# Performance work log

Measured on AMD Instinct MI355X. Metric: run time of the kernel, lower is better.

Reference implementation:

```python
import jax, jax.numpy as jnp
from jax import lax
import numpy as np

B, N, H, K = 64, 256, 1024, 3  # batch, num_proposals, hidden_dim, conv kernel size
LN_EPS = 1e-5


def setup_inputs() -> dict:
    key = jax.random.key(0)
    k1, k2, k3 = jax.random.split(key, 3)
    scale = 1.0 / np.sqrt(H)
    return {
        "f": jax.random.normal(k1, (B, N, H), dtype=jnp.float32),
        "k": jax.random.normal(k2, (B, N, H), dtype=jnp.float32),
        "W_lin": jax.random.normal(k3, (N * K, H), dtype=jnp.float32) * scale,
        "b_lin": jnp.zeros((N * K,), dtype=jnp.float32),
        "ln_gamma": jnp.ones((H,), dtype=jnp.float32),
        "ln_beta": jnp.zeros((H,), dtype=jnp.float32),
    }


def _conv_one(x, w):
    # x: [N, H] (channels, length); w: [N_out, N_in, K]
    # PyTorch F.conv1d is cross-correlation, same as lax conv with no flip.
    y = lax.conv_general_dilated(
        x[None], w, window_strides=(1,), padding="SAME",
        dimension_numbers=("NCH", "OIH", "NCH"))
    return y[0]  # [N, H]


def reference(f, k, W_lin, b_lin, ln_gamma, ln_beta):
    # Dynamic weight generation: [B, N, H] -> [B, N, N*K] -> [B, N, N, K]
    weight = jnp.einsum("bnh,oh->bno", f, W_lin) + b_lin
    weight = weight.reshape(B, N, N, K)
    # Per-sample dynamic conv1d over the hidden dim (batched via vmap)
    out = jax.vmap(_conv_one)(k, weight)  # [B, N, H]
    # LayerNorm over hidden dim
    mu = jnp.mean(out, axis=-1, keepdims=True)
    var = jnp.var(out, axis=-1, keepdims=True)
    out = (out - mu) * lax.rsqrt(var + LN_EPS) * ln_gamma + ln_beta
    return out
```

## Files before the change

kernel.cpp:

```cpp
#include <hip/hip_runtime.h>
#include <math.h>

#define Bsz 64
#define Nn  256
#define Hh  1024
#define NK  768

typedef __bf16 bf16;
typedef bf16 bf16x4 __attribute__((ext_vector_type(4)));
typedef bf16 bf16x8 __attribute__((ext_vector_type(8)));
typedef float floatx4 __attribute__((ext_vector_type(4)));

#define KT_ROWS   1026
#define KT_BSTRIDE (KT_ROWS * 256)

__device__ __forceinline__ void gl_lds16(const bf16* g, bf16* l) {
    __builtin_amdgcn_global_load_lds(
        (__attribute__((address_space(1))) void*)(g),
        (__attribute__((address_space(3))) void*)(l), 16, 0, 0);
}
__device__ __forceinline__ void gl_lds16f(const float* g, float* l) {
    __builtin_amdgcn_global_load_lds(
        (__attribute__((address_space(1))) void*)(g),
        (__attribute__((address_space(3))) void*)(l), 16, 0, 0);
}

__global__ __launch_bounds__(256) void transpose_kernel(
    const float* __restrict__ kin, bf16* __restrict__ kTp)
{
    __shared__ float Tf[64 * 128];
    const int tid = threadIdx.x;
    const int bid = blockIdx.x;
    const int hb = bid & 7, ib = (bid >> 3) & 3, b = bid >> 5;
    const int i0 = ib * 64, h0 = hb * 128;
    const float* src = kin + ((size_t)b << 18);
    bf16* dstb = kTp + (size_t)b * KT_BSTRIDE;

    if (hb == 0 && ib == 0) {
        dstb[tid] = (bf16)0.f;
        dstb[(size_t)1025 * 256 + tid] = (bf16)0.f;
    }
    #pragma unroll
    for (int j = 0; j < 8; ++j) {
        int c  = tid + j * 256;
        int il = c >> 5;
        int hq = (c & 31) ^ j;
        gl_lds16f(src + (size_t)(i0 + il) * Hh + h0 + hq * 4, Tf + c * 4);
    }
    __syncthreads();
    const int q = tid & 7;
    #pragma unroll
    for (int p = 0; p < 4; ++p) {
        int hl = (tid >> 3) + p * 32;
        bf16x8 o;
        #pragma unroll
        for (int j = 0; j < 8; ++j) {
            int i = q * 8 + j;
            float v = Tf[i * 128 + (((hl >> 2) ^ q) << 2) + (hl & 3)];
            o[j] = (bf16)v;
        }
        *(bf16x8*)&dstb[(size_t)(h0 + hl + 1) * 256 + i0 + q * 8] = o;
    }
}

__global__ __launch_bounds__(256) void cast_kernel(
    const float* __restrict__ f, const float* __restrict__ wl,
    bf16* __restrict__ fbf, bf16* __restrict__ wlbf)
{
    const int STR = 524288;
    const int u0  = blockIdx.x * 256 + threadIdx.x;
    float4 a[8];
    #pragma unroll
    for (int k = 0; k < 4; ++k) {
        const float4* s4 = (const float4*)f + ((size_t)(u0 + k * STR) * 2);
        a[2 * k]     = s4[0];
        a[2 * k + 1] = s4[1];
    }
    float4 b0, b1;
    const bool doW = (u0 < 98304);
    if (doW) {
        const float4* s4 = (const float4*)wl + ((size_t)u0 * 2);
        b0 = s4[0];
        b1 = s4[1];
    }
    __builtin_amdgcn_sched_barrier(0);
    #pragma unroll
    for (int k = 0; k < 4; ++k) {
        bf16x8 o = {(bf16)a[2*k].x, (bf16)a[2*k].y, (bf16)a[2*k].z, (bf16)a[2*k].w,
                    (bf16)a[2*k+1].x, (bf16)a[2*k+1].y, (bf16)a[2*k+1].z, (bf16)a[2*k+1].w};
        ((bf16x8*)fbf)[u0 + k * STR] = o;
    }
    if (doW) {
        bf16x8 o = {(bf16)b0.x, (bf16)b0.y, (bf16)b0.z, (bf16)b0.w,
                    (bf16)b1.x, (bf16)b1.y, (bf16)b1.z, (bf16)b1.w};
        ((bf16x8*)wlbf)[u0] = o;
    }
}

__global__ __launch_bounds__(256) void gemm1_mfma(
    const bf16* __restrict__ A,
    const bf16* __restrict__ Bw,
    const float* __restrict__ bias,
    bf16* __restrict__ wgt3)
{
    __shared__ bf16 smem[25600];
    bf16* As = smem;
    bf16* Bs = smem + 8192;
    const int tid  = threadIdx.x;
    const int wave = tid >> 6, lane = tid & 63;
    const int row0 = blockIdx.y * 128;
    const int col0 = blockIdx.x * 192;

    const bf16* gA[4]; bf16* lA[4];
    #pragma unroll
    for (int j = 0; j < 4; ++j) {
        int s = tid + j * 256;
        int reg = s >> 9, rem = s & 511, row = rem >> 2, quad = rem & 3;
        gA[j] = A + (size_t)(row0 + row) * Hh + reg * 32 + quad * 8;
        lA[j] = As + s * 8;
    }
    const bf16* gB[6]; bf16* lB[6];
    #pragma unroll
    for (int j = 0; j < 6; ++j) {
        int s = tid + j * 256;
        int reg = s / 768, rem = s - reg * 768, row = rem >> 2, quad = rem & 3;
        gB[j] = Bw + (size_t)(col0 + row) * Hh + reg * 32 + quad * 8;
        lB[j] = Bs + s * 8;
    }

    const int wm = wave & 1, wn = wave >> 1;
    const int fm = lane & 15, koct = (lane >> 4) * 8;

    floatx4 zero = {0.f, 0.f, 0.f, 0.f};
    floatx4 acc[4][6];
    #pragma unroll
    for (int i = 0; i < 4; ++i)
        #pragma unroll
        for (int j = 0; j < 6; ++j) acc[i][j] = zero;

    for (int k0 = 0; k0 < Hh; k0 += 64) {
        #pragma unroll
        for (int j = 0; j < 4; ++j) gl_lds16(gA[j] + k0, lA[j]);
        #pragma unroll
        for (int j = 0; j < 6; ++j) gl_lds16(gB[j] + k0, lB[j]);
        __syncthreads();
        #pragma unroll
        for (int q = 0; q < 2; ++q) {
            bf16x8 af[4], bfr[6];
            #pragma unroll
            for (int mt = 0; mt < 4; ++mt)
                af[mt] = *(const bf16x8*)&As[q * 4096 + (wm * 64 + mt * 16 + fm) * 32 + koct];
            #pragma unroll
            for (int nt = 0; nt < 6; ++nt)
                bfr[nt] = *(const bf16x8*)&Bs[q * 6144 + (wn * 96 + nt * 16 + fm) * 32 + koct];
            #pragma unroll
            for (int mt = 0; mt < 4; ++mt)
                #pragma unroll
                for (int nt = 0; nt < 6; ++nt)
                    acc[mt][nt] = __builtin_amdgcn_mfma_f32_16x16x32_bf16(
                        af[mt], bfr[nt], acc[mt][nt], 0, 0, 0);
        }
        __syncthreads();
    }

    const int b  = row0 >> 8;
    const int nb = row0 & 255;
    bf16* Cs = smem;
    #pragma unroll
    for (int nt = 0; nt < 6; ++nt) {
        int c = wn * 96 + nt * 16 + fm;
        float bl = bias[col0 + c];
        #pragma unroll
        for (int mt = 0; mt < 4; ++mt) {
            int rb = wm * 64 + mt * 16 + (lane >> 4) * 4;
            #pragma unroll
            for (int r = 0; r < 4; ++r)
                Cs[(rb + r) * 200 + c] = (bf16)(acc[mt][nt][r] + bl);
        }
    }
    __syncthreads();
    const int i0 = blockIdx.x * 64;
    #pragma unroll
    for (int j = 0; j < 12; ++j) {
        int s = tid + j * 256;
        int t = s >> 10, rem = s & 1023, n = rem >> 3, q8 = rem & 7;
        bf16x8 v;
        #pragma unroll
        for (int u = 0; u < 8; ++u)
            v[u] = Cs[n * 200 + (q8 * 8 + u) * 3 + t];
        *(bf16x8*)&wgt3[((size_t)(b * 3 + t) << 16) + ((size_t)(nb + n) << 8) + i0 + q8 * 8] = v;
    }
}

__global__ __launch_bounds__(256, 3) void conv_mfma(
    const bf16* __restrict__ kTp,
    const bf16* __restrict__ wgt3,
    bf16* __restrict__ cbuf)
{
    __shared__ bf16 As[6144];
    __shared__ bf16 Ks[8256];
    const int tid  = threadIdx.x;
    const int wave = tid >> 6, lane = tid & 63;
    const int b  = blockIdx.z;
    const int o0 = blockIdx.y * 64;
    const int h0 = blockIdx.x * 256;
    const int wm = wave & 1, wn = wave >> 1;
    const int fm = lane & 15, koct = (lane >> 4) * 8;

    const bf16* gA[3]; bf16* lA[3];
    #pragma unroll
    for (int j = 0; j < 3; ++j) {
        int s = tid + j * 256;
        int t = s >> 8, rem = s & 255, o = rem >> 2, iq = rem & 3;
        gA[j] = wgt3 + ((size_t)(b * 3 + t) << 16) + ((size_t)(o0 + o) << 8) + iq * 8;
        lA[j] = As + s * 8;
    }
    const bf16* kb = kTp + (size_t)b * KT_BSTRIDE;
    const bf16* gK[4]; bf16* lK[4];
    #pragma unroll
    for (int j = 0; j < 4; ++j) {
        int s = tid + j * 256;
        int r = s >> 2, quad = s & 3;
        gK[j] = kb + (size_t)(h0 + r) * 256 + quad * 8;
        lK[j] = Ks + s * 8;
    }

    floatx4 zero = {0.f, 0.f, 0.f, 0.f};
    floatx4 acc[2][8];
    #pragma unroll
    for (int i = 0; i < 2; ++i)
        #pragma unroll
        for (int j = 0; j < 8; ++j) acc[i][j] = zero;

    for (int ic = 0; ic < 8; ++ic) {
        const int i0 = ic * 32;
        __syncthreads();
        #pragma unroll
        for (int j = 0; j < 3; ++j) gl_lds16(gA[j] + i0, lA[j]);
        #pragma unroll
        for (int j = 0; j < 4; ++j) gl_lds16(gK[j] + i0, lK[j]);
        if (tid < 8) {
            int r = 256 + (tid >> 2), q = tid & 3;
            bf16x8 v = *(const bf16x8*)&kb[(size_t)(h0 + r) * 256 + i0 + q * 8];
            *(bf16x8*)&Ks[r * 32 + q * 8] = v;
        }
        __syncthreads();
        #pragma unroll
        for (int t = 0; t < 3; ++t) {
            bf16x8 af[2], bfr[8];
            #pragma unroll
            for (int mt = 0; mt < 2; ++mt)
                af[mt] = *(const bf16x8*)&As[t * 2048 + (wm * 32 + mt * 16 + fm) * 32 + koct];
            #pragma unroll
            for (int nt = 0; nt < 8; ++nt)
                bfr[nt] = *(const bf16x8*)&Ks[(wn * 128 + nt * 16 + fm + t) * 32 + koct];
            #pragma unroll
            for (int mt = 0; mt < 2; ++mt)
                #pragma unroll
                for (int nt = 0; nt < 8; ++nt)
                    acc[mt][nt] = __builtin_amdgcn_mfma_f32_16x16x32_bf16(
                        af[mt], bfr[nt], acc[mt][nt], 0, 0, 0);
        }
    }

    #pragma unroll
    for (int mt = 0; mt < 2; ++mt) {
        int o = o0 + wm * 32 + mt * 16 + (lane >> 4) * 4;
        #pragma unroll
        for (int nt = 0; nt < 8; ++nt) {
            int h = h0 + wn * 128 + nt * 16 + fm;
            #pragma unroll
            for (int r = 0; r < 4; ++r)
                cbuf[((size_t)(b * 256 + o + r) << 10) + h] = (bf16)acc[mt][nt][r];
        }
    }
}

__global__ __launch_bounds__(256) void ln_kernel(
    const bf16* __restrict__ cbuf, const float* __restrict__ gamma,
    const float* __restrict__ beta, float* __restrict__ out)
{
    const int tid  = threadIdx.x;
    const int t    = tid & 127;
    const int half = tid >> 7;
    bf16x8 v[4];
    #pragma unroll
    for (int it = 0; it < 4; ++it) {
        const int row = (blockIdx.x << 3) + it * 2 + half;
        v[it] = *(const bf16x8*)(cbuf + ((size_t)row << 10) + t * 8);
    }
    float4 g0  = ((const float4*)gamma)[t * 2];
    float4 g1  = ((const float4*)gamma)[t * 2 + 1];
    float4 be0 = ((const float4*)beta)[t * 2];
    float4 be1 = ((const float4*)beta)[t * 2 + 1];
    __shared__ float r1[2][4], r2[2][4];
    #pragma unroll
    for (int it = 0; it < 4; ++it) {
        const int row = (blockIdx.x << 3) + it * 2 + half;
        float x[8];
        float s1 = 0.f, s2 = 0.f;
        #pragma unroll
        for (int u = 0; u < 8; ++u) {
            x[u] = (float)v[it][u];
            s1 += x[u];
            s2 += x[u] * x[u];
        }
        #pragma unroll
        for (int m = 1; m < 64; m <<= 1) {
            s1 += __shfl_xor(s1, m, 64);
            s2 += __shfl_xor(s2, m, 64);
        }
        const int p = it & 1;
        if ((tid & 63) == 0) { r1[p][tid >> 6] = s1; r2[p][tid >> 6] = s2; }
        __syncthreads();
        float S1 = r1[p][2 * half] + r1[p][2 * half + 1];
        float S2 = r2[p][2 * half] + r2[p][2 * half + 1];
        float mu   = S1 * (1.0f / 1024.0f);
        float var  = S2 * (1.0f / 1024.0f) - mu * mu;
        float rstd = rsqrtf(var + 1e-5f);
        float4 o0, o1;
        o0.x = (x[0] - mu) * rstd * g0.x + be0.x;
        o0.y = (x[1] - mu) * rstd * g0.y + be0.y;
        o0.z = (x[2] - mu) * rstd * g0.z + be0.z;
        o0.w = (x[3] - mu) * rstd * g0.w + be0.w;
        o1.x = (x[4] - mu) * rstd * g1.x + be1.x;
        o1.y = (x[5] - mu) * rstd * g1.y + be1.y;
        o1.z = (x[6] - mu) * rstd * g1.z + be1.z;
        o1.w = (x[7] - mu) * rstd * g1.w + be1.w;
        float* orow = out + ((size_t)row << 10) + t * 8;
        ((float4*)orow)[0] = o0;
        ((float4*)orow)[1] = o1;
    }
}

extern "C" void kernel_launch(void* const* d_in, const int* in_sizes, int n_in,
                              void* d_out, int out_size, void* d_ws, size_t ws_size,
                              hipStream_t stream) {
    const float* f     = (const float*)d_in[0];
    const float* kin   = (const float*)d_in[1];
    const float* W_lin = (const float*)d_in[2];
    const float* b_lin = (const float*)d_in[3];
    const float* gamma = (const float*)d_in[4];
    const float* beta  = (const float*)d_in[5];
    float* out = (float*)d_out;

    char* ws = (char*)d_ws;
    bf16* fbf  = (bf16*)(ws);
    bf16* cbuf = (bf16*)(ws);
    bf16* wlbf = (bf16*)(ws + 33554432);
    bf16* kTp  = (bf16*)(ws + 35127296);
    bf16* wgt3 = (bf16*)(ws + 68747264);

    transpose_kernel<<<2048, 256, 0, stream>>>(kin, kTp);
    cast_kernel<<<2048, 256, 0, stream>>>(f, W_lin, fbf, wlbf);
    gemm1_mfma<<<dim3(4, 128), 256, 0, stream>>>(fbf, wlbf, b_lin, wgt3);
    conv_mfma<<<dim3(4, 4, 64), 256, 0, stream>>>(kTp, wgt3, cbuf);
    ln_kernel<<<2048, 256, 0, stream>>>(cbuf, gamma, beta, out);
}
```

Before: 274.9 us.

## Double-buffer LDS tiles in gemm1 and conv kernels to overlap loads with MFMA

Both the weight-generation GEMM and the dynamic conv kernel now use two LDS buffers. The next K-slice is prefetched with global_load_lds while MFMAs run on the current one, which leaves one barrier per iteration instead of two. The GEMM K step shrinks from 64 to 32 to fit two buffers in the existing shared array. The conv kernel doubles its LDS, lowers its occupancy hint from 3 to 2 blocks, and prefetches its halo rows through registers. Lower occupancy and more loop iterations could offset the overlap gain.

```diff
diff --git a/kernel.cpp b/kernel.cpp
--- a/kernel.cpp
+++ b/kernel.cpp
@@ -104,28 +104,26 @@
     bf16* __restrict__ wgt3)
 {
     __shared__ bf16 smem[25600];
-    bf16* As = smem;
-    bf16* Bs = smem + 8192;
     const int tid  = threadIdx.x;
     const int wave = tid >> 6, lane = tid & 63;
     const int row0 = blockIdx.y * 128;
     const int col0 = blockIdx.x * 192;
 
-    const bf16* gA[4]; bf16* lA[4];
-    #pragma unroll
-    for (int j = 0; j < 4; ++j) {
-        int s = tid + j * 256;
-        int reg = s >> 9, rem = s & 511, row = rem >> 2, quad = rem & 3;
-        gA[j] = A + (size_t)(row0 + row) * Hh + reg * 32 + quad * 8;
-        lA[j] = As + s * 8;
-    }
-    const bf16* gB[6]; bf16* lB[6];
-    #pragma unroll
-    for (int j = 0; j < 6; ++j) {
-        int s = tid + j * 256;
-        int reg = s / 768, rem = s - reg * 768, row = rem >> 2, quad = rem & 3;
-        gB[j] = Bw + (size_t)(col0 + row) * Hh + reg * 32 + quad * 8;
-        lB[j] = Bs + s * 8;
+    const bf16* gA[2]; int lA[2];
+    #pragma unroll
+    for (int j = 0; j < 2; ++j) {
+        int s = tid + j * 256;
+        int row = s >> 2, quad = s & 3;
+        gA[j] = A + (size_t)(row0 + row) * Hh + quad * 8;
+        lA[j] = s * 8;
+    }
+    const bf16* gB[3]; int lB[3];
+    #pragma unroll
+    for (int j = 0; j < 3; ++j) {
+        int s = tid + j * 256;
+        int row = s >> 2, quad = s & 3;
+        gB[j] = Bw + (size_t)(col0 + row) * Hh + quad * 8;
+        lB[j] = 4096 + s * 8;
     }
 
     const int wm = wave & 1, wn = wave >> 1;
@@ -138,29 +136,38 @@
         #pragma unroll
         for (int j = 0; j < 6; ++j) acc[i][j] = zero;
 
-    for (int k0 = 0; k0 < Hh; k0 += 64) {
-        #pragma unroll
-        for (int j = 0; j < 4; ++j) gl_lds16(gA[j] + k0, lA[j]);
-        #pragma unroll
-        for (int j = 0; j < 6; ++j) gl_lds16(gB[j] + k0, lB[j]);
+    #pragma unroll
+    for (int j = 0; j < 2; ++j) gl_lds16(gA[j], &smem[lA[j]]);
+    #pragma unroll
+    for (int j = 0; j < 3; ++j) gl_lds16(gB[j], &smem[lB[j]]);
+    __syncthreads();
+
+    int cur = 0;
+    for (int hs = 0; hs < 32; ++hs) {
+        if (hs < 31) {
+            const int ko = (hs + 1) * 32;
+            const int nb = (cur ^ 1) * 10240;
+            #pragma unroll
+            for (int j = 0; j < 2; ++j) gl_lds16(gA[j] + ko, &smem[nb + lA[j]]);
+            #pragma unroll
+            for (int j = 0; j < 3; ++j) gl_lds16(gB[j] + ko, &smem[nb + lB[j]]);
+        }
+        const int cb = cur * 10240;
+        bf16x8 af[4], bfr[6];
+        #pragma unroll
+        for (int mt = 0; mt < 4; ++mt)
+            af[mt] = *(const bf16x8*)&smem[cb + (wm * 64 + mt * 16 + fm) * 32 + koct];
+        #pragma unroll
+        for (int nt = 0; nt < 6; ++nt)
+            bfr[nt] = *(const bf16x8*)&smem[cb + 4096 + (wn * 96 + nt * 16 + fm) * 32 + koct];
+        #pragma unroll
+        for (int mt = 0; mt < 4; ++mt)
+            #pragma unroll
+            for (int nt = 0; nt < 6; ++nt)
+                acc[mt][nt] = __builtin_amdgcn_mfma_f32_16x16x32_bf16(
+                    af[mt], bfr[nt], acc[mt][nt], 0, 0, 0);
         __syncthreads();
-        #pragma unroll
-        for (int q = 0; q < 2; ++q) {
-            bf16x8 af[4], bfr[6];
-            #pragma unroll
-            for (int mt = 0; mt < 4; ++mt)
-                af[mt] = *(const bf16x8*)&As[q * 4096 + (wm * 64 + mt * 16 + fm) * 32 + koct];
-            #pragma unroll
-            for (int nt = 0; nt < 6; ++nt)
-                bfr[nt] = *(const bf16x8*)&Bs[q * 6144 + (wn * 96 + nt * 16 + fm) * 32 + koct];
-            #pragma unroll
-            for (int mt = 0; mt < 4; ++mt)
-                #pragma unroll
-                for (int nt = 0; nt < 6; ++nt)
-                    acc[mt][nt] = __builtin_amdgcn_mfma_f32_16x16x32_bf16(
-                        af[mt], bfr[nt], acc[mt][nt], 0, 0, 0);
-        }
-        __syncthreads();
+        cur ^= 1;
     }
 
     const int b  = row0 >> 8;
@@ -192,13 +199,13 @@
     }
 }
 
-__global__ __launch_bounds__(256, 3) void conv_mfma(
+__global__ __launch_bounds__(256, 2) void conv_mfma(
     const bf16* __restrict__ kTp,
     const bf16* __restrict__ wgt3,
     bf16* __restrict__ cbuf)
 {
-    __shared__ bf16 As[6144];
-    __shared__ bf16 Ks[8256];
+    __shared__ bf16 As[2][6144];
+    __shared__ bf16 Ks[2][8256];
     const int tid  = threadIdx.x;
     const int wave = tid >> 6, lane = tid & 63;
     const int b  = blockIdx.z;
@@ -207,23 +214,25 @@
     const int wm = wave & 1, wn = wave >> 1;
     const int fm = lane & 15, koct = (lane >> 4) * 8;
 
-    const bf16* gA[3]; bf16* lA[3];
+    const bf16* gA[3]; int lA[3];
     #pragma unroll
     for (int j = 0; j < 3; ++j) {
         int s = tid + j * 256;
         int t = s >> 8, rem = s & 255, o = rem >> 2, iq = rem & 3;
         gA[j] = wgt3 + ((size_t)(b * 3 + t) << 16) + ((size_t)(o0 + o) << 8) + iq * 8;
-        lA[j] = As + s * 8;
+        lA[j] = s * 8;
     }
     const bf16* kb = kTp + (size_t)b * KT_BSTRIDE;
-    const bf16* gK[4]; bf16* lK[4];
+    const bf16* gK[4]; int lK[4];
     #pragma unroll
     for (int j = 0; j < 4; ++j) {
         int s = tid + j * 256;
         int r = s >> 2, quad = s & 3;
         gK[j] = kb + (size_t)(h0 + r) * 256 + quad * 8;
-        lK[j] = Ks + s * 8;
-    }
+        lK[j] = s * 8;
+    }
+    const bf16* gH = kb + (size_t)(h0 + 256 + (tid >> 2)) * 256 + (tid & 3) * 8;
+    const int lH = (256 + (tid >> 2)) * 32 + (tid & 3) * 8;
 
     floatx4 zero = {0.f, 0.f, 0.f, 0.f};
     floatx4 acc[2][8];
@@ -232,28 +241,35 @@
         #pragma unroll
         for (int j = 0; j < 8; ++j) acc[i][j] = zero;
 
+    bf16x8 hv;
+    if (tid < 8) hv = *(const bf16x8*)gH;
+    #pragma unroll
+    for (int j = 0; j < 3; ++j) gl_lds16(gA[j], &As[0][lA[j]]);
+    #pragma unroll
+    for (int j = 0; j < 4; ++j) gl_lds16(gK[j], &Ks[0][lK[j]]);
+    if (tid < 8) *(bf16x8*)&Ks[0][lH] = hv;
+    __syncthreads();
+
+    int cur = 0;
     for (int ic = 0; ic < 8; ++ic) {
-        const int i0 = ic * 32;
-        __syncthreads();
-        #pragma unroll
-        for (int j = 0; j < 3; ++j) gl_lds16(gA[j] + i0, lA[j]);
-        #pragma unroll
-        for (int j = 0; j < 4; ++j) gl_lds16(gK[j] + i0, lK[j]);
-        if (tid < 8) {
-            int r = 256 + (tid >> 2), q = tid & 3;
-            bf16x8 v = *(const bf16x8*)&kb[(size_t)(h0 + r) * 256 + i0 + q * 8];
-            *(bf16x8*)&Ks[r * 32 + q * 8] = v;
-        }
-        __syncthreads();
+        const int nxo = (ic + 1) * 32;
+        bf16x8 hn;
+        if (ic < 7) {
+            if (tid < 8) hn = *(const bf16x8*)(gH + nxo);
+            #pragma unroll
+            for (int j = 0; j < 3; ++j) gl_lds16(gA[j] + nxo, &As[cur ^ 1][lA[j]]);
+            #pragma unroll
+            for (int j = 0; j < 4; ++j) gl_lds16(gK[j] + nxo, &Ks[cur ^ 1][lK[j]]);
+        }
         #pragma unroll
         for (int t = 0; t < 3; ++t) {
             bf16x8 af[2], bfr[8];
             #pragma unroll
             for (int mt = 0; mt < 2; ++mt)
-                af[mt] = *(const bf16x8*)&As[t * 2048 + (wm * 32 + mt * 16 + fm) * 32 + koct];
+                af[mt] = *(const bf16x8*)&As[cur][t * 2048 + (wm * 32 + mt * 16 + fm) * 32 + koct];
             #pragma unroll
             for (int nt = 0; nt < 8; ++nt)
-                bfr[nt] = *(const bf16x8*)&Ks[(wn * 128 + nt * 16 + fm + t) * 32 + koct];
+                bfr[nt] = *(const bf16x8*)&Ks[cur][(wn * 128 + nt * 16 + fm + t) * 32 + koct];
             #pragma unroll
             for (int mt = 0; mt < 2; ++mt)
                 #pragma unroll
@@ -261,6 +277,9 @@
                     acc[mt][nt] = __builtin_amdgcn_mfma_f32_16x16x32_bf16(
                         af[mt], bfr[nt], acc[mt][nt], 0, 0, 0);
         }
+        if (ic < 7 && tid < 8) *(bf16x8*)&Ks[cur ^ 1][lH] = hn;
+        __syncthreads();
+        cur ^= 1;
     }
 
     #pragma unroll
```

Result: no change. 274.3 us (-0.2%).

## Fuse fp32-to-bf16 cast into GEMM loads and remap grids for XCD locality

Applied to the files above, without the earlier changes.

Removes the separate cast kernel. The GEMM now loads fp32 f and W_lin directly into registers, converts them to bf16 and stores them to LDS, which saves a full write and re-read of the bf16 copies. Both the GEMM and the conv kernels switch to a 1-D grid with XCD-aware block remapping so blocks sharing a batch land on the same XCD and reuse its L2. The conv tile in h is halved, with fewer accumulators and the occupancy hint dropped, which gives more blocks. The cost is that the direct-to-LDS async loads become synchronous register loads with no double buffering in the GEMM.

```diff
diff --git a/kernel.cpp b/kernel.cpp
--- a/kernel.cpp
+++ b/kernel.cpp
@@ -63,69 +63,33 @@
     }
 }
 
-__global__ __launch_bounds__(256) void cast_kernel(
-    const float* __restrict__ f, const float* __restrict__ wl,
-    bf16* __restrict__ fbf, bf16* __restrict__ wlbf)
-{
-    const int STR = 524288;
-    const int u0  = blockIdx.x * 256 + threadIdx.x;
-    float4 a[8];
-    #pragma unroll
-    for (int k = 0; k < 4; ++k) {
-        const float4* s4 = (const float4*)f + ((size_t)(u0 + k * STR) * 2);
-        a[2 * k]     = s4[0];
-        a[2 * k + 1] = s4[1];
-    }
-    float4 b0, b1;
-    const bool doW = (u0 < 98304);
-    if (doW) {
-        const float4* s4 = (const float4*)wl + ((size_t)u0 * 2);
-        b0 = s4[0];
-        b1 = s4[1];
-    }
-    __builtin_amdgcn_sched_barrier(0);
-    #pragma unroll
-    for (int k = 0; k < 4; ++k) {
-        bf16x8 o = {(bf16)a[2*k].x, (bf16)a[2*k].y, (bf16)a[2*k].z, (bf16)a[2*k].w,
-                    (bf16)a[2*k+1].x, (bf16)a[2*k+1].y, (bf16)a[2*k+1].z, (bf16)a[2*k+1].w};
-        ((bf16x8*)fbf)[u0 + k * STR] = o;
-    }
-    if (doW) {
-        bf16x8 o = {(bf16)b0.x, (bf16)b0.y, (bf16)b0.z, (bf16)b0.w,
-                    (bf16)b1.x, (bf16)b1.y, (bf16)b1.z, (bf16)b1.w};
-        ((bf16x8*)wlbf)[u0] = o;
-    }
-}
-
 __global__ __launch_bounds__(256) void gemm1_mfma(
-    const bf16* __restrict__ A,
-    const bf16* __restrict__ Bw,
+    const float* __restrict__ A,
+    const float* __restrict__ Bw,
     const float* __restrict__ bias,
     bf16* __restrict__ wgt3)
 {
     __shared__ bf16 smem[25600];
-    bf16* As = smem;
-    bf16* Bs = smem + 8192;
     const int tid  = threadIdx.x;
     const int wave = tid >> 6, lane = tid & 63;
-    const int row0 = blockIdx.y * 128;
-    const int col0 = blockIdx.x * 192;
-
-    const bf16* gA[4]; bf16* lA[4];
-    #pragma unroll
-    for (int j = 0; j < 4; ++j) {
-        int s = tid + j * 256;
-        int reg = s >> 9, rem = s & 511, row = rem >> 2, quad = rem & 3;
-        gA[j] = A + (size_t)(row0 + row) * Hh + reg * 32 + quad * 8;
-        lA[j] = As + s * 8;
-    }
-    const bf16* gB[6]; bf16* lB[6];
-    #pragma unroll
-    for (int j = 0; j < 6; ++j) {
-        int s = tid + j * 256;
-        int reg = s / 768, rem = s - reg * 768, row = rem >> 2, quad = rem & 3;
-        gB[j] = Bw + (size_t)(col0 + row) * Hh + reg * 32 + quad * 8;
-        lB[j] = Bs + s * 8;
+    const int bid = blockIdx.x;
+    const int xcd = bid & 7, loc = bid >> 3;
+    const int ry  = (xcd << 4) | (loc >> 2);
+    const int cx  = loc & 3;
+    const int row0 = ry * 128;
+    const int col0 = cx * 192;
+
+    size_t offA[8];
+    #pragma unroll
+    for (int j = 0; j < 8; ++j) {
+        int c = tid + j * 256, row = c >> 4, kq = c & 15;
+        offA[j] = (size_t)(row0 + row) * Hh + kq * 4;
+    }
+    size_t offB[12];
+    #pragma unroll
+    for (int j = 0; j < 12; ++j) {
+        int c = tid + j * 256, row = c >> 4, kq = c & 15;
+        offB[j] = (size_t)(col0 + row) * Hh + kq * 4;
     }
 
     const int wm = wave & 1, wn = wave >> 1;
@@ -139,20 +103,35 @@
         for (int j = 0; j < 6; ++j) acc[i][j] = zero;
 
     for (int k0 = 0; k0 < Hh; k0 += 64) {
-        #pragma unroll
-        for (int j = 0; j < 4; ++j) gl_lds16(gA[j] + k0, lA[j]);
-        #pragma unroll
-        for (int j = 0; j < 6; ++j) gl_lds16(gB[j] + k0, lB[j]);
+        float4 av[8];
+        #pragma unroll
+        for (int j = 0; j < 8; ++j) av[j] = *(const float4*)&A[offA[j] + k0];
+        float4 bv[12];
+        #pragma unroll
+        for (int j = 0; j < 12; ++j) bv[j] = *(const float4*)&Bw[offB[j] + k0];
+        __syncthreads();
+        #pragma unroll
+        for (int j = 0; j < 8; ++j) {
+            int c = tid + j * 256;
+            bf16x4 o = {(bf16)av[j].x, (bf16)av[j].y, (bf16)av[j].z, (bf16)av[j].w};
+            *(bf16x4*)&smem[c * 4] = o;
+        }
+        #pragma unroll
+        for (int j = 0; j < 12; ++j) {
+            int c = tid + j * 256;
+            bf16x4 o = {(bf16)bv[j].x, (bf16)bv[j].y, (bf16)bv[j].z, (bf16)bv[j].w};
+            *(bf16x4*)&smem[8192 + c * 4] = o;
+        }
         __syncthreads();
         #pragma unroll
         for (int q = 0; q < 2; ++q) {
             bf16x8 af[4], bfr[6];
             #pragma unroll
             for (int mt = 0; mt < 4; ++mt)
-                af[mt] = *(const bf16x8*)&As[q * 4096 + (wm * 64 + mt * 16 + fm) * 32 + koct];
+                af[mt] = *(const bf16x8*)&smem[(wm * 64 + mt * 16 + fm) * 64 + q * 32 + koct];
             #pragma unroll
             for (int nt = 0; nt < 6; ++nt)
-                bfr[nt] = *(const bf16x8*)&Bs[q * 6144 + (wn * 96 + nt * 16 + fm) * 32 + koct];
+                bfr[nt] = *(const bf16x8*)&smem[8192 + (wn * 96 + nt * 16 + fm) * 64 + q * 32 + koct];
             #pragma unroll
             for (int mt = 0; mt < 4; ++mt)
                 #pragma unroll
@@ -160,8 +139,8 @@
                     acc[mt][nt] = __builtin_amdgcn_mfma_f32_16x16x32_bf16(
                         af[mt], bfr[nt], acc[mt][nt], 0, 0, 0);
         }
-        __syncthreads();
-    }
+    }
+    __syncthreads();
 
     const int b  = row0 >> 8;
     const int nb = row0 & 255;
@@ -179,7 +158,7 @@
         }
     }
     __syncthreads();
-    const int i0 = blockIdx.x * 64;
+    const int i0 = cx * 64;
     #pragma unroll
     for (int j = 0; j < 12; ++j) {
         int s = tid + j * 256;
@@ -192,18 +171,21 @@
     }
 }
 
-__global__ __launch_bounds__(256, 3) void conv_mfma(
+__global__ __launch_bounds__(256) void conv_mfma(
     const bf16* __restrict__ kTp,
     const bf16* __restrict__ wgt3,
     bf16* __restrict__ cbuf)
 {
     __shared__ bf16 As[6144];
-    __shared__ bf16 Ks[8256];
+    __shared__ bf16 Ks[4160];
     const int tid  = threadIdx.x;
     const int wave = tid >> 6, lane = tid & 63;
-    const int b  = blockIdx.z;
-    const int o0 = blockIdx.y * 64;
-    const int h0 = blockIdx.x * 256;
+    const int bid = blockIdx.x;
+    const int xcd = bid & 7, loc = bid >> 3;
+    const int b   = (xcd << 3) | (loc >> 5);
+    const int rem = loc & 31;
+    const int o0  = (rem >> 3) * 64;
+    const int h0  = (rem & 7) * 128;
     const int wm = wave & 1, wn = wave >> 1;
     const int fm = lane & 15, koct = (lane >> 4) * 8;
 
@@ -211,26 +193,28 @@
     #pragma unroll
     for (int j = 0; j < 3; ++j) {
         int s = tid + j * 256;
-        int t = s >> 8, rem = s & 255, o = rem >> 2, iq = rem & 3;
+        int t = s >> 8, r2 = s & 255, o = r2 >> 2, iq = r2 & 3;
         gA[j] = wgt3 + ((size_t)(b * 3 + t) << 16) + ((size_t)(o0 + o) << 8) + iq * 8;
         lA[j] = As + s * 8;
     }
     const bf16* kb = kTp + (size_t)b * KT_BSTRIDE;
-    const bf16* gK[4]; bf16* lK[4];
-    #pragma unroll
-    for (int j = 0; j < 4; ++j) {
+    const bf16* gK[2]; bf16* lK[2];
+    #pragma unroll
+    for (int j = 0; j < 2; ++j) {
         int s = tid + j * 256;
         int r = s >> 2, quad = s & 3;
         gK[j] = kb + (size_t)(h0 + r) * 256 + quad * 8;
         lK[j] = Ks + s * 8;
     }
+    const bf16* gH = kb + (size_t)(h0 + 128 + (tid >> 2)) * 256 + (tid & 3) * 8;
+    const int lH = (128 + (tid >> 2)) * 32 + (tid & 3) * 8;
 
     floatx4 zero = {0.f, 0.f, 0.f, 0.f};
-    floatx4 acc[2][8];
+    floatx4 acc[2][4];
     #pragma unroll
     for (int i = 0; i < 2; ++i)
         #pragma unroll
-        for (int j = 0; j < 8; ++j) acc[i][j] = zero;
+        for (int j = 0; j < 4; ++j) acc[i][j] = zero;
 
     for (int ic = 0; ic < 8; ++ic) {
         const int i0 = ic * 32;
@@ -238,26 +222,25 @@
         #pragma unroll
         for (int j = 0; j < 3; ++j) gl_lds16(gA[j] + i0, lA[j]);
         #pragma unroll
-        for (int j = 0; j < 4; ++j) gl_lds16(gK[j] + i0, lK[j]);
+        for (int j = 0; j < 2; ++j) gl_lds16(gK[j] + i0, lK[j]);
         if (tid < 8) {
-            int r = 256 + (tid >> 2), q = tid & 3;
-            bf16x8 v = *(const bf16x8*)&kb[(size_t)(h0 + r) * 256 + i0 + q * 8];
-            *(bf16x8*)&Ks[r * 32 + q * 8] = v;
+            bf16x8 v = *(const bf16x8*)(gH + i0);
+            *(bf16x8*)&Ks[lH] = v;
         }
         __syncthreads();
         #pragma unroll
         for (int t = 0; t < 3; ++t) {
-            bf16x8 af[2], bfr[8];
+            bf16x8 af[2], bfr[4];
             #pragma unroll
             for (int mt = 0; mt < 2; ++mt)
                 af[mt] = *(const bf16x8*)&As[t * 2048 + (wm * 32 + mt * 16 + fm) * 32 + koct];
             #pragma unroll
-            for (int nt = 0; nt < 8; ++nt)
-                bfr[nt] = *(const bf16x8*)&Ks[(wn * 128 + nt * 16 + fm + t) * 32 + koct];
+            for (int nt = 0; nt < 4; ++nt)
+                bfr[nt] = *(const bf16x8*)&Ks[(wn * 64 + nt * 16 + fm + t) * 32 + koct];
             #pragma unroll
             for (int mt = 0; mt < 2; ++mt)
                 #pragma unroll
-                for (int nt = 0; nt < 8; ++nt)
+                for (int nt = 0; nt < 4; ++nt)
                     acc[mt][nt] = __builtin_amdgcn_mfma_f32_16x16x32_bf16(
                         af[mt], bfr[nt], acc[mt][nt], 0, 0, 0);
         }
@@ -267,8 +250,8 @@
     for (int mt = 0; mt < 2; ++mt) {
         int o = o0 + wm * 32 + mt * 16 + (lane >> 4) * 4;
         #pragma unroll
-        for (int nt = 0; nt < 8; ++nt) {
-            int h = h0 + wn * 128 + nt * 16 + fm;
+        for (int nt = 0; nt < 4; ++nt) {
+            int h = h0 + wn * 64 + nt * 16 + fm;
             #pragma unroll
             for (int r = 0; r < 4; ++r)
                 cbuf[((size_t)(b * 256 + o + r) << 10) + h] = (bf16)acc[mt][nt][r];
@@ -345,15 +328,12 @@
     float* out = (float*)d_out;
 
     char* ws = (char*)d_ws;
-    bf16* fbf  = (bf16*)(ws);
     bf16* cbuf = (bf16*)(ws);
-    bf16* wlbf = (bf16*)(ws + 33554432);
     bf16* kTp  = (bf16*)(ws + 35127296);
     bf16* wgt3 = (bf16*)(ws + 68747264);
 
     transpose_kernel<<<2048, 256, 0, stream>>>(kin, kTp);
-    cast_kernel<<<2048, 256, 0, stream>>>(f, W_lin, fbf, wlbf);
-    gemm1_mfma<<<dim3(4, 128), 256, 0, stream>>>(fbf, wlbf, b_lin, wgt3);
-    conv_mfma<<<dim3(4, 4, 64), 256, 0, stream>>>(kTp, wgt3, cbuf);
+    gemm1_mfma<<<512, 256, 0, stream>>>(f, W_lin, b_lin, wgt3);
+    conv_mfma<<<2048, 256, 0, stream>>>(kTp, wgt3, cbuf);
     ln_kernel<<<2048, 256, 0, stream>>>(cbuf, gamma, beta, out);
 }
```

Measured after the change: 259.8 us. 5.5% less time.
